# Optimization experiments

Hardware: AMD Instinct MI355X
Metric: run time of the kernel (lower is better)

The kernel has to match this reference:

```python
import jax, jax.numpy as jnp
import numpy as np

DIM = 256; WS = 8; HEADS = 8; HD = DIM // HEADS; SCALE = HD ** -0.5; MLP_HIDDEN = 1024
B = 8; H = 128; W = 128


def setup_inputs() -> dict:
    key = jax.random.key(0)
    ks = jax.random.split(key, 16)
    def nrm(k, shape, s=0.02):
        return jax.random.normal(k, shape, jnp.float32) * s
    # relative position index (same construction as torch buffer)
    coords = np.stack(np.meshgrid(np.arange(WS), np.arange(WS), indexing='ij')).reshape(2, -1)
    rel = (coords[:, :, None] - coords[:, None, :]).transpose(1, 2, 0).astype(np.int64)
    rel[..., 0] += WS - 1; rel[..., 1] += WS - 1; rel[..., 0] *= 2 * WS - 1
    rel_idx = jnp.asarray(rel.sum(-1), jnp.int32)  # (64,64) in [0,225)
    return dict(
        x=nrm(ks[0], (B, H, W, DIM), 1.0),
        rel_table=nrm(ks[1], ((2 * WS - 1) ** 2, HEADS)),
        qkv_w=nrm(ks[2], (3 * DIM, DIM)), qkv_b=nrm(ks[3], (3 * DIM,)),
        qkv2_w=nrm(ks[4], (3 * DIM, DIM)), qkv2_b=nrm(ks[5], (3 * DIM,)),
        proj_ln_w=jnp.ones((DIM,), jnp.float32), proj_ln_b=jnp.zeros((DIM,), jnp.float32),
        proj_w=nrm(ks[6], (DIM, DIM)), proj_b=nrm(ks[7], (DIM,)),
        proj2_ln_w=jnp.ones((DIM,), jnp.float32), proj2_ln_b=jnp.zeros((DIM,), jnp.float32),
        proj2_w=nrm(ks[8], (DIM, DIM)), proj2_b=nrm(ks[9], (DIM,)),
        norm1_w=jnp.ones((DIM,), jnp.float32), norm1_b=jnp.zeros((DIM,), jnp.float32),
        norm2_w=jnp.ones((DIM,), jnp.float32), norm2_b=jnp.zeros((DIM,), jnp.float32),
        fc1_w=nrm(ks[10], (MLP_HIDDEN, DIM)), fc1_b=nrm(ks[11], (MLP_HIDDEN,)),
        fc2_w=nrm(ks[12], (DIM, MLP_HIDDEN)), fc2_b=nrm(ks[13], (DIM,)),
        rel_idx=rel_idx,
    )


def _ln(x, w, b):
    mu = x.mean(-1, keepdims=True)
    var = ((x - mu) ** 2).mean(-1, keepdims=True)
    return (x - mu) / jnp.sqrt(var + 1e-5) * w + b


def _mha(tokens, wqkv, bqkv, bias=None):
    Bt, N, C = tokens.shape
    qkv = (tokens @ wqkv.T + bqkv).reshape(Bt, N, 3, HEADS, HD).transpose(2, 0, 3, 1, 4)
    q, k, v = qkv[0] * SCALE, qkv[1], qkv[2]
    attn = jnp.einsum('bhnd,bhmd->bhnm', q, k)
    if bias is not None:
        attn = attn + bias  # (1,heads,N,N) relative position bias
    attn = jax.nn.softmax(attn, axis=-1)
    out = jnp.einsum('bhnm,bhmd->bhnd', attn, v)
    return out.transpose(0, 2, 1, 3).reshape(Bt, N, C)


def _pos_sine(h, w, c):
    # PositionEmbeddingSine(normalize=True), mask all-zero -> cumsum = 1..h / 1..w
    npf = c // 2
    scale = 2.0 * np.pi; eps = 1e-5
    y = jnp.arange(1, h + 1, dtype=jnp.float32); y = y / (y[-1] + eps) * scale
    xw = jnp.arange(1, w + 1, dtype=jnp.float32); xw = xw / (xw[-1] + eps) * scale
    dim_t = 10000.0 ** ((2.0 * (jnp.arange(npf) // 2)) / npf)
    def enc(e):  # (L,) -> (L,npf) interleaved sin/cos
        p = e[:, None] / dim_t
        return jnp.stack([jnp.sin(p[:, 0::2]), jnp.cos(p[:, 1::2])], axis=-1).reshape(e.shape[0], npf)
    py = enc(y); px = enc(xw)
    return jnp.concatenate([jnp.broadcast_to(py[:, None, :], (h, w, npf)),
                            jnp.broadcast_to(px[None, :, :], (h, w, npf))], axis=-1)  # (h,w,c)


def _upsample_ac(x, oh, ow):
    # bilinear, align_corners=True; x: (B,h,w,C)
    Bn, h, w, C = x.shape
    def idx(n, o):
        s = jnp.linspace(0.0, n - 1.0, o)
        i0 = jnp.floor(s).astype(jnp.int32)
        i1 = jnp.minimum(i0 + 1, n - 1)
        return i0, i1, s - i0
    y0, y1, ty = idx(h, oh)
    x = x[:, y0] * (1 - ty)[None, :, None, None] + x[:, y1] * ty[None, :, None, None]
    x0, x1, tx = idx(w, ow)
    x = x[:, :, x0] * (1 - tx)[None, None, :, None] + x[:, :, x1] * tx[None, None, :, None]
    return x


def reference(x, rel_table, qkv_w, qkv_b, qkv2_w, qkv2_b,
              proj_ln_w, proj_ln_b, proj_w, proj_b,
              proj2_ln_w, proj2_ln_b, proj2_w, proj2_b,
              norm1_w, norm1_b, norm2_w, norm2_b,
              fc1_w, fc1_b, fc2_w, fc2_b, rel_idx):
    Bn, Hh, Ww, C = x.shape  # H,W divisible by WS -> padding is a no-op
    nh, nw = Hh // WS, Ww // WS
    N = WS * WS
    shortcut = x
    # window partition -> (B*nh*nw, N, C)
    xw = x.reshape(Bn, nh, WS, nw, WS, C).transpose(0, 1, 3, 2, 4, 5).reshape(-1, N, C)
    bias = rel_table[rel_idx.reshape(-1)].reshape(N, N, HEADS).transpose(2, 0, 1)[None]
    xw = _mha(xw, qkv_w, qkv_b, bias)
    xw = xw.reshape(Bn, nh, nw, WS, WS, C).transpose(0, 1, 3, 2, 4, 5).reshape(Bn, Hh, Ww, C)
    x = shortcut + xw
    x = x + (_ln(x, proj_ln_w, proj_ln_b) @ proj_w.T + proj_b)
    shortcut = x
    # global branch: avgpool each window, sine pos enc, full attention, bilinear upsample
    xg = x.reshape(Bn, nh, WS, nw, WS, C).mean(axis=(2, 4))  # (B,nh,nw,C)
    xg = xg + _pos_sine(nh, nw, C)[None]
    xg = _mha(xg.reshape(Bn, nh * nw, C), qkv2_w, qkv2_b).reshape(Bn, nh, nw, C)
    xg = _upsample_ac(xg, Hh, Ww)
    x = shortcut + xg
    x = x + (_ln(x, proj2_ln_w, proj2_ln_b) @ proj2_w.T + proj2_b)
    h = _ln(x, norm1_w, norm1_b)
    h = jax.nn.gelu(h @ fc1_w.T + fc1_b, approximate=False) @ fc2_w.T + fc2_b
    x = x + h
    return _ln(x, norm2_w, norm2_b)
```

## Files before the change

### kernel.cpp

```cpp
#include <hip/hip_runtime.h>
#include <math.h>

#define DEV __device__ __forceinline__

constexpr int NTOK = 131072;
constexpr int TOKS_PER_B = 16384;
constexpr float SCALE_F = 0.17677669529663687f;

typedef float f32x4 __attribute__((ext_vector_type(4)));
typedef __bf16 bf16x8 __attribute__((ext_vector_type(8)));
typedef unsigned short us8 __attribute__((ext_vector_type(8)));

DEV float gelu1(float v) { return 0.5f * v * (1.f + erff(v * 0.7071067811865476f)); }
DEV unsigned short f2bf(float x) { __bf16 b = (__bf16)x; return __builtin_bit_cast(unsigned short, b); }
DEV float bfh2f(unsigned short h) { return __builtin_bit_cast(float, ((unsigned)h) << 16); }

__global__ void cvtw_k(const float* __restrict__ w, unsigned short* __restrict__ dst, int n) {
  const int i = (blockIdx.x * 256 + threadIdx.x) * 4;
  float4 v = *(const float4*)(w + i);
  ushort4 h, l;
  h.x = f2bf(v.x); l.x = f2bf(v.x - bfh2f(h.x));
  h.y = f2bf(v.y); l.y = f2bf(v.y - bfh2f(h.y));
  h.z = f2bf(v.z); l.z = f2bf(v.z - bfh2f(h.z));
  h.w = f2bf(v.w); l.w = f2bf(v.w - bfh2f(h.w));
  *(ushort4*)(dst + i) = h;
  *(ushort4*)(dst + n + i) = l;
}

template <bool LNA, bool RES, bool GELU>
__launch_bounds__(256)
__global__ void gemm_mfma(const float* __restrict__ A, const unsigned short* __restrict__ Wp,
                          const float* __restrict__ bias, float* out,
                          const float* __restrict__ stats,
                          const float* __restrict__ lnw, const float* __restrict__ lnb,
                          int M, int N, int K) {
  __shared__ unsigned short Ah[64][40], Al[64][40];
  __shared__ unsigned short Wh[256][40], Wl[256][40];
  const int t = threadIdx.x;
  const int lane = t & 63, wid = t >> 6;
  const int m0 = blockIdx.x * 64, n0 = blockIdx.y * 256;
  const unsigned short* Whp = Wp;
  const unsigned short* Wlp = Wp + (size_t)N * K;

  f32x4 acc[4][4];
#pragma unroll
  for (int i = 0; i < 4; ++i)
#pragma unroll
    for (int j = 0; j < 4; ++j) acc[i][j] = (f32x4){0.f, 0.f, 0.f, 0.f};

  const int fr = lane & 15, ko = (lane >> 4) * 8;

  for (int k0 = 0; k0 < K; k0 += 32) {
#pragma unroll
    for (int it = 0; it < 2; ++it) {
      const int id = t + it * 256;
      const int r = id >> 3, cg = id & 7;
      float4 v = *(const float4*)(A + (size_t)(m0 + r) * K + k0 + cg * 4);
      if (LNA) {
        const float mu = stats[(size_t)(m0 + r) * 2];
        const float rs = stats[(size_t)(m0 + r) * 2 + 1];
        float4 w4 = *(const float4*)(lnw + k0 + cg * 4);
        float4 b4 = *(const float4*)(lnb + k0 + cg * 4);
        v.x = (v.x - mu) * rs * w4.x + b4.x; v.y = (v.y - mu) * rs * w4.y + b4.y;
        v.z = (v.z - mu) * rs * w4.z + b4.z; v.w = (v.w - mu) * rs * w4.w + b4.w;
      }
      ushort4 h, l;
      h.x = f2bf(v.x); l.x = f2bf(v.x - bfh2f(h.x));
      h.y = f2bf(v.y); l.y = f2bf(v.y - bfh2f(h.y));
      h.z = f2bf(v.z); l.z = f2bf(v.z - bfh2f(h.z));
      h.w = f2bf(v.w); l.w = f2bf(v.w - bfh2f(h.w));
      *(ushort4*)&Ah[r][cg * 4] = h;
      *(ushort4*)&Al[r][cg * 4] = l;
    }
#pragma unroll
    for (int it = 0; it < 4; ++it) {
      const int id = t + it * 256;
      const int rn = id >> 2, kc = (id & 3) * 8;
      const size_t goff = (size_t)(n0 + rn) * K + k0 + kc;
      *(us8*)&Wh[rn][kc] = *(const us8*)(Whp + goff);
      *(us8*)&Wl[rn][kc] = *(const us8*)(Wlp + goff);
    }
    __syncthreads();
    bf16x8 ah[4], al[4], bh[4], bl[4];
#pragma unroll
    for (int i = 0; i < 4; ++i) {
      ah[i] = __builtin_bit_cast(bf16x8, *(const us8*)&Ah[i * 16 + fr][ko]);
      al[i] = __builtin_bit_cast(bf16x8, *(const us8*)&Al[i * 16 + fr][ko]);
      bh[i] = __builtin_bit_cast(bf16x8, *(const us8*)&Wh[wid * 64 + i * 16 + fr][ko]);
      bl[i] = __builtin_bit_cast(bf16x8, *(const us8*)&Wl[wid * 64 + i * 16 + fr][ko]);
    }
#pragma unroll
    for (int i = 0; i < 4; ++i)
#pragma unroll
      for (int j = 0; j < 4; ++j) {
        acc[i][j] = __builtin_amdgcn_mfma_f32_16x16x32_bf16(ah[i], bh[j], acc[i][j], 0, 0, 0);
        acc[i][j] = __builtin_amdgcn_mfma_f32_16x16x32_bf16(ah[i], bl[j], acc[i][j], 0, 0, 0);
        acc[i][j] = __builtin_amdgcn_mfma_f32_16x16x32_bf16(al[i], bh[j], acc[i][j], 0, 0, 0);
      }
    __syncthreads();
  }
  const int orow = (lane >> 4) * 4;
#pragma unroll
  for (int i = 0; i < 4; ++i)
#pragma unroll
    for (int j = 0; j < 4; ++j) {
      const int col = n0 + wid * 64 + j * 16 + fr;
      const float b = bias[col];
#pragma unroll
      for (int r = 0; r < 4; ++r) {
        const int row = m0 + i * 16 + orow + r;
        float v = acc[i][j][r] + b;
        if (GELU) v = gelu1(v);
        float* p = out + (size_t)row * N + col;
        if (RES) v += *p;
        *p = v;
      }
    }
}

__global__ void winattn_k(const float* __restrict__ qkv, const float* __restrict__ xin,
                          float* __restrict__ X, const float* __restrict__ rel_table,
                          const int* __restrict__ rel_idx, int b0) {
  __shared__ float klds[64][36];
  __shared__ float vlds[64][36];
  const int b_rel = blockIdx.x >> 11;
  const int rest = blockIdx.x & 2047;
  const int widx = rest >> 3, h = rest & 7;
  const int wy = widx >> 4, wx = widx & 15;
  const int r = threadIdx.x;
  const int tl = (wy * 8 + (r >> 3)) * 128 + wx * 8 + (r & 7);
  const float* qr = qkv + ((size_t)b_rel * TOKS_PER_B + tl) * 768 + h * 32;
  float q[32];
#pragma unroll
  for (int j4 = 0; j4 < 8; ++j4) {
    float4 v = *(const float4*)(qr + j4 * 4);
    q[j4*4+0] = v.x * SCALE_F; q[j4*4+1] = v.y * SCALE_F;
    q[j4*4+2] = v.z * SCALE_F; q[j4*4+3] = v.w * SCALE_F;
  }
#pragma unroll
  for (int j4 = 0; j4 < 8; ++j4) {
    *(float4*)&klds[r][j4 * 4] = *(const float4*)(qr + 256 + j4 * 4);
    *(float4*)&vlds[r][j4 * 4] = *(const float4*)(qr + 512 + j4 * 4);
  }
  __syncthreads();
  float s[64];
  const int* ri = rel_idx + r * 64;
#pragma unroll
  for (int m = 0; m < 64; ++m) {
    float acc = 0.f;
#pragma unroll
    for (int j4 = 0; j4 < 8; ++j4) {
      float4 k4 = *(const float4*)&klds[m][j4 * 4];
      acc += q[j4*4+0]*k4.x + q[j4*4+1]*k4.y + q[j4*4+2]*k4.z + q[j4*4+3]*k4.w;
    }
    s[m] = acc + rel_table[ri[m] * 8 + h];
  }
  float mx = s[0];
#pragma unroll
  for (int m = 1; m < 64; ++m) mx = fmaxf(mx, s[m]);
  float sum = 0.f;
#pragma unroll
  for (int m = 0; m < 64; ++m) { s[m] = __expf(s[m] - mx); sum += s[m]; }
  const float inv = 1.f / sum;
  float o[32];
#pragma unroll
  for (int j = 0; j < 32; ++j) o[j] = 0.f;
#pragma unroll
  for (int m = 0; m < 64; ++m) {
    const float p = s[m];
#pragma unroll
    for (int j4 = 0; j4 < 8; ++j4) {
      float4 v4 = *(const float4*)&vlds[m][j4 * 4];
      o[j4*4+0] += p * v4.x; o[j4*4+1] += p * v4.y;
      o[j4*4+2] += p * v4.z; o[j4*4+3] += p * v4.w;
    }
  }
  const size_t go = (size_t)((b0 + b_rel) * TOKS_PER_B + tl) * 256 + h * 32;
#pragma unroll
  for (int j4 = 0; j4 < 8; ++j4) {
    float4 xi = *(const float4*)(xin + go + j4 * 4);
    float4 rr;
    rr.x = o[j4*4+0] * inv + xi.x; rr.y = o[j4*4+1] * inv + xi.y;
    rr.z = o[j4*4+2] * inv + xi.z; rr.w = o[j4*4+3] * inv + xi.w;
    *(float4*)(X + go + j4 * 4) = rr;
  }
}

__global__ void lnstats_k(const float* __restrict__ X, float* __restrict__ stats) {
  const int lane = threadIdx.x & 63;
  const int wave = threadIdx.x >> 6;
  for (int tok = blockIdx.x * 4 + wave; tok < NTOK; tok += gridDim.x * 4) {
    float4 v = *(const float4*)(X + (size_t)tok * 256 + lane * 4);
    float s = v.x + v.y + v.z + v.w;
    float q = v.x*v.x + v.y*v.y + v.z*v.z + v.w*v.w;
#pragma unroll
    for (int off = 32; off > 0; off >>= 1) {
      s += __shfl_xor(s, off, 64);
      q += __shfl_xor(q, off, 64);
    }
    if (lane == 0) {
      const float m = s * (1.f / 256.f);
      const float var = q * (1.f / 256.f) - m * m;
      stats[(size_t)tok * 2] = m;
      stats[(size_t)tok * 2 + 1] = 1.f / sqrtf(var + 1e-5f);
    }
  }
}

__global__ void finalln_k(float* X, const float* __restrict__ w, const float* __restrict__ b) {
  const int lane = threadIdx.x & 63;
  const int wave = threadIdx.x >> 6;
  for (int tok = blockIdx.x * 4 + wave; tok < NTOK; tok += gridDim.x * 4) {
    float* p = X + (size_t)tok * 256 + lane * 4;
    float4 v = *(const float4*)p;
    float s = v.x + v.y + v.z + v.w;
    float q = v.x*v.x + v.y*v.y + v.z*v.z + v.w*v.w;
#pragma unroll
    for (int off = 32; off > 0; off >>= 1) {
      s += __shfl_xor(s, off, 64);
      q += __shfl_xor(q, off, 64);
    }
    const float m = s * (1.f / 256.f);
    const float var = q * (1.f / 256.f) - m * m;
    const float rs = 1.f / sqrtf(var + 1e-5f);
    float4 w4 = *(const float4*)(w + lane * 4);
    float4 b4 = *(const float4*)(b + lane * 4);
    v.x = (v.x - m) * rs * w4.x + b4.x; v.y = (v.y - m) * rs * w4.y + b4.y;
    v.z = (v.z - m) * rs * w4.z + b4.z; v.w = (v.w - m) * rs * w4.w + b4.w;
    *(float4*)p = v;
  }
}

__global__ void poolsine_k(const float* __restrict__ X, float* __restrict__ G0) {
  const int c = threadIdx.x;
  const int wx = blockIdx.x & 15, wy = (blockIdx.x >> 4) & 15, b = blockIdx.x >> 8;
  const float* base = X + ((size_t)(b * 128 + wy * 8) * 128 + wx * 8) * 256 + c;
  float s = 0.f;
  for (int ry = 0; ry < 8; ++ry)
#pragma unroll
    for (int rx = 0; rx < 8; ++rx) s += base[((size_t)ry * 128 + rx) * 256];
  s *= (1.f / 64.f);
  const float sc = 6.283185307179586f / (16.f + 1e-5f);
  const int cc = c & 127;
  const float d = powf(10000.f, (float)(cc >> 1) * (1.f / 64.f));
  const float e = ((c < 128 ? (float)(wy + 1) : (float)(wx + 1)) * sc) / d;
  const float pos = (cc & 1) ? cosf(e) : sinf(e);
  G0[(size_t)blockIdx.x * 256 + c] = s + pos;
}

__global__ void gattn_k(const float* __restrict__ G1, float* __restrict__ G2) {
  const int b = blockIdx.x, h = blockIdx.y, n = threadIdx.x;
  const float* qp = G1 + ((size_t)b * 256 + n) * 768 + h * 32;
  float q[32];
#pragma unroll
  for (int j4 = 0; j4 < 8; ++j4) {
    float4 v = *(const float4*)(qp + j4 * 4);
    q[j4*4+0] = v.x * SCALE_F; q[j4*4+1] = v.y * SCALE_F;
    q[j4*4+2] = v.z * SCALE_F; q[j4*4+3] = v.w * SCALE_F;
  }
  const float* kb = G1 + (size_t)b * 256 * 768 + 256 + h * 32;
  const float* vb = kb + 256;
  float out[32];
#pragma unroll
  for (int j = 0; j < 32; ++j) out[j] = 0.f;
  float mx = -3.4e38f, l = 0.f;
  for (int m = 0; m < 256; ++m) {
    const float* kr = kb + (size_t)m * 768;
    float s = 0.f;
#pragma unroll
    for (int j4 = 0; j4 < 8; ++j4) {
      float4 k4 = *(const float4*)(kr + j4 * 4);
      s += q[j4*4+0]*k4.x + q[j4*4+1]*k4.y + q[j4*4+2]*k4.z + q[j4*4+3]*k4.w;
    }
    const float mn = fmaxf(mx, s);
    const float corr = __expf(mx - mn);
    const float p = __expf(s - mn);
    l = l * corr + p;
    const float* vr = vb + (size_t)m * 768;
#pragma unroll
    for (int j4 = 0; j4 < 8; ++j4) {
      float4 v4 = *(const float4*)(vr + j4 * 4);
      out[j4*4+0] = out[j4*4+0]*corr + p*v4.x; out[j4*4+1] = out[j4*4+1]*corr + p*v4.y;
      out[j4*4+2] = out[j4*4+2]*corr + p*v4.z; out[j4*4+3] = out[j4*4+3]*corr + p*v4.w;
    }
    mx = mn;
  }
  const float inv = 1.f / l;
  float* op = G2 + ((size_t)b * 256 + n) * 256 + h * 32;
#pragma unroll
  for (int j4 = 0; j4 < 8; ++j4) {
    float4 r;
    r.x = out[j4*4+0]*inv; r.y = out[j4*4+1]*inv;
    r.z = out[j4*4+2]*inv; r.w = out[j4*4+3]*inv;
    *(float4*)(op + j4 * 4) = r;
  }
}

__global__ void upadd_k(float* __restrict__ X, const float* __restrict__ G2,
                        float* __restrict__ stats) {
  const int c = threadIdx.x;
  const int tok = blockIdx.x;
  const int j = tok & 127, i = (tok >> 7) & 127, b = tok >> 14;
  const float sy = i * (15.f / 127.f);
  const float sx = j * (15.f / 127.f);
  const int y0 = (int)sy; const float ty = sy - y0; const int y1 = min(y0 + 1, 15);
  const int x0 = (int)sx; const float tx = sx - x0; const int x1 = min(x0 + 1, 15);
  const float* gb = G2 + (size_t)b * 256 * 256;
  const float v00 = gb[((size_t)(y0 * 16 + x0)) * 256 + c];
  const float v01 = gb[((size_t)(y0 * 16 + x1)) * 256 + c];
  const float v10 = gb[((size_t)(y1 * 16 + x0)) * 256 + c];
  const float v11 = gb[((size_t)(y1 * 16 + x1)) * 256 + c];
  const float vy0 = v00 * (1.f - ty) + v10 * ty;
  const float vy1 = v01 * (1.f - ty) + v11 * ty;
  const float val = X[(size_t)tok * 256 + c] + vy0 * (1.f - tx) + vy1 * tx;
  X[(size_t)tok * 256 + c] = val;
  float s = val, q = val * val;
#pragma unroll
  for (int off = 32; off > 0; off >>= 1) {
    s += __shfl_xor(s, off, 64);
    q += __shfl_xor(q, off, 64);
  }
  __shared__ float red[8];
  const int lane = c & 63, wave = c >> 6;
  if (lane == 0) { red[wave * 2] = s; red[wave * 2 + 1] = q; }
  __syncthreads();
  if (c == 0) {
    const float S = red[0] + red[2] + red[4] + red[6];
    const float Q = red[1] + red[3] + red[5] + red[7];
    const float m = S * (1.f / 256.f);
    const float var = Q * (1.f / 256.f) - m * m;
    stats[(size_t)tok * 2] = m;
    stats[(size_t)tok * 2 + 1] = 1.f / sqrtf(var + 1e-5f);
  }
}

extern "C" void kernel_launch(void* const* d_in, const int* in_sizes, int n_in,
                              void* d_out, int out_size, void* d_ws, size_t ws_size,
                              hipStream_t stream) {
  const float* x          = (const float*)d_in[0];
  const float* rel_table  = (const float*)d_in[1];
  const float* qkv_w      = (const float*)d_in[2];
  const float* qkv_b      = (const float*)d_in[3];
  const float* qkv2_w     = (const float*)d_in[4];
  const float* qkv2_b     = (const float*)d_in[5];
  const float* proj_ln_w  = (const float*)d_in[6];
  const float* proj_ln_b  = (const float*)d_in[7];
  const float* proj_w     = (const float*)d_in[8];
  const float* proj_b     = (const float*)d_in[9];
  const float* proj2_ln_w = (const float*)d_in[10];
  const float* proj2_ln_b = (const float*)d_in[11];
  const float* proj2_w    = (const float*)d_in[12];
  const float* proj2_b    = (const float*)d_in[13];
  const float* norm1_w    = (const float*)d_in[14];
  const float* norm1_b    = (const float*)d_in[15];
  const float* norm2_w    = (const float*)d_in[16];
  const float* norm2_b    = (const float*)d_in[17];
  const float* fc1_w      = (const float*)d_in[18];
  const float* fc1_b      = (const float*)d_in[19];
  const float* fc2_w      = (const float*)d_in[20];
  const float* fc2_b      = (const float*)d_in[21];
  const int*   rel_idx    = (const int*)d_in[22];

  float* X = (float*)d_out;
  char* wsb = (char*)d_ws;
  float* stats = (float*)wsb;
  float* G0 = (float*)(wsb + (size_t)1048576);
  float* G1 = G0 + (size_t)2048 * 256;
  float* G2 = G1 + (size_t)2048 * 768;
  unsigned short* WCVT = (unsigned short*)(G2 + (size_t)2048 * 256);
  float* BIG = (float*)((char*)WCVT + (size_t)4194304);
  const size_t fixed = (size_t)((char*)BIG - wsb);
  const size_t avail = ws_size > fixed ? ws_size - fixed : 0;

  unsigned short* w_qkv  = WCVT;
  unsigned short* w_qkv2 = WCVT + 393216;
  unsigned short* w_proj = WCVT + 786432;
  unsigned short* w_proj2= WCVT + 917504;
  unsigned short* w_fc1  = WCVT + 1048576;
  unsigned short* w_fc2  = WCVT + 1572864;
  cvtw_k<<<192, 256, 0, stream>>>(qkv_w,   w_qkv,   196608);
  cvtw_k<<<192, 256, 0, stream>>>(qkv2_w,  w_qkv2,  196608);
  cvtw_k<<<64,  256, 0, stream>>>(proj_w,  w_proj,   65536);
  cvtw_k<<<64,  256, 0, stream>>>(proj2_w, w_proj2,  65536);
  cvtw_k<<<256, 256, 0, stream>>>(fc1_w,   w_fc1,   262144);
  cvtw_k<<<256, 256, 0, stream>>>(fc2_w,   w_fc2,   262144);

  int st = 8192;
  if (avail >= (size_t)65536 * 1024 * 4) st = 65536;
  else if (avail >= (size_t)32768 * 1024 * 4) st = 32768;
  else if (avail >= (size_t)16384 * 1024 * 4) st = 16384;
  const bool one_shot_qkv = avail >= (size_t)NTOK * 768 * 4;

  if (one_shot_qkv) {
    gemm_mfma<false, false, false><<<dim3(NTOK / 64, 3), 256, 0, stream>>>(
        x, w_qkv, qkv_b, BIG, nullptr, nullptr, nullptr, NTOK, 768, 256);
    winattn_k<<<16384, 64, 0, stream>>>(BIG, x, X, rel_table, rel_idx, 0);
  } else {
    for (int b = 0; b < 8; ++b) {
      gemm_mfma<false, false, false><<<dim3(TOKS_PER_B / 64, 3), 256, 0, stream>>>(
          x + (size_t)b * TOKS_PER_B * 256, w_qkv, qkv_b, BIG,
          nullptr, nullptr, nullptr, TOKS_PER_B, 768, 256);
      winattn_k<<<2048, 64, 0, stream>>>(BIG, x, X, rel_table, rel_idx, b);
    }
  }
  lnstats_k<<<1024, 256, 0, stream>>>(X, stats);
  gemm_mfma<true, true, false><<<dim3(NTOK / 64, 1), 256, 0, stream>>>(
      X, w_proj, proj_b, X, stats, proj_ln_w, proj_ln_b, NTOK, 256, 256);
  poolsine_k<<<2048, 256, 0, stream>>>(X, G0);
  gemm_mfma<false, false, false><<<dim3(32, 3), 256, 0, stream>>>(
      G0, w_qkv2, qkv2_b, G1, nullptr, nullptr, nullptr, 2048, 768, 256);
  gattn_k<<<dim3(8, 8), 256, 0, stream>>>(G1, G2);
  upadd_k<<<NTOK, 256, 0, stream>>>(X, G2, stats);
  gemm_mfma<true, true, false><<<dim3(NTOK / 64, 1), 256, 0, stream>>>(
      X, w_proj2, proj2_b, X, stats, proj2_ln_w, proj2_ln_b, NTOK, 256, 256);
  lnstats_k<<<1024, 256, 0, stream>>>(X, stats);
  for (int s0 = 0; s0 < NTOK; s0 += st) {
    gemm_mfma<true, false, true><<<dim3(st / 64, 4), 256, 0, stream>>>(
        X + (size_t)s0 * 256, w_fc1, fc1_b, BIG, stats + (size_t)s0 * 2,
        norm1_w, norm1_b, st, 1024, 256);
    gemm_mfma<false, true, false><<<dim3(st / 64, 1), 256, 0, stream>>>(
        BIG, w_fc2, fc2_b, X + (size_t)s0 * 256, nullptr, nullptr, nullptr,
        st, 256, 1024);
  }
  finalln_k<<<1024, 256, 0, stream>>>(X, norm2_w, norm2_b);
}
```

Before: 2.129 ms.

## Switch GEMMs to fp16 split-weight MFMA and store intermediates in half

Replaces the three-pass bf16 hi/lo split GEMM with fp16 MFMA that uses a single fp16 activation and split fp16 weights, so each tile needs two MFMAs instead of three and one A staging buffer instead of two. The QKV and fc1 intermediate buffers are now written in fp16, which halves the traffic of the large intermediates and lets fc2 read half-precision A directly. Window attention now packs four windows per 256-thread block and reads fp16 K/V from LDS, and the fc chunk size grows because the buffers are smaller. The risks are lower accuracy from rounding activations to fp16 (range and precision) and possible overflow of the fp16 intermediates.

Result: slower. 2.408 ms (+13.1%).

```diff
diff --git a/kernel.cpp b/kernel.cpp
--- a/kernel.cpp
+++ b/kernel.cpp
@@ -8,38 +8,37 @@
 constexpr float SCALE_F = 0.17677669529663687f;
 
 typedef float f32x4 __attribute__((ext_vector_type(4)));
-typedef __bf16 bf16x8 __attribute__((ext_vector_type(8)));
+typedef _Float16 half8 __attribute__((ext_vector_type(8)));
 typedef unsigned short us8 __attribute__((ext_vector_type(8)));
 
 DEV float gelu1(float v) { return 0.5f * v * (1.f + erff(v * 0.7071067811865476f)); }
-DEV unsigned short f2bf(float x) { __bf16 b = (__bf16)x; return __builtin_bit_cast(unsigned short, b); }
-DEV float bfh2f(unsigned short h) { return __builtin_bit_cast(float, ((unsigned)h) << 16); }
-
-__global__ void cvtw_k(const float* __restrict__ w, unsigned short* __restrict__ dst, int n) {
+DEV unsigned short f2h(float x) { _Float16 h = (_Float16)x; return __builtin_bit_cast(unsigned short, h); }
+DEV float h2f(unsigned short u) { return (float)__builtin_bit_cast(_Float16, u); }
+
+__global__ void cvtw16_k(const float* __restrict__ w, unsigned short* __restrict__ dst, int n) {
   const int i = (blockIdx.x * 256 + threadIdx.x) * 4;
   float4 v = *(const float4*)(w + i);
   ushort4 h, l;
-  h.x = f2bf(v.x); l.x = f2bf(v.x - bfh2f(h.x));
-  h.y = f2bf(v.y); l.y = f2bf(v.y - bfh2f(h.y));
-  h.z = f2bf(v.z); l.z = f2bf(v.z - bfh2f(h.z));
-  h.w = f2bf(v.w); l.w = f2bf(v.w - bfh2f(h.w));
+  h.x = f2h(v.x); l.x = f2h(v.x - h2f(h.x));
+  h.y = f2h(v.y); l.y = f2h(v.y - h2f(h.y));
+  h.z = f2h(v.z); l.z = f2h(v.z - h2f(h.z));
+  h.w = f2h(v.w); l.w = f2h(v.w - h2f(h.w));
   *(ushort4*)(dst + i) = h;
   *(ushort4*)(dst + n + i) = l;
 }
 
-template <bool LNA, bool RES, bool GELU>
+template <int AMODE, bool RES, bool GELU, bool OUTH>
 __launch_bounds__(256)
-__global__ void gemm_mfma(const float* __restrict__ A, const unsigned short* __restrict__ Wp,
-                          const float* __restrict__ bias, float* out,
-                          const float* __restrict__ stats,
-                          const float* __restrict__ lnw, const float* __restrict__ lnb,
-                          int M, int N, int K) {
-  __shared__ unsigned short Ah[64][40], Al[64][40];
+__global__ void gemm16(const void* __restrict__ Ain, const unsigned short* __restrict__ Wp,
+                       const float* __restrict__ bias, void* __restrict__ outv,
+                       const float* __restrict__ stats,
+                       const float* __restrict__ lnw, const float* __restrict__ lnb,
+                       int M, int N, int K) {
+  __shared__ unsigned short As[64][40];
   __shared__ unsigned short Wh[256][40], Wl[256][40];
   const int t = threadIdx.x;
   const int lane = t & 63, wid = t >> 6;
   const int m0 = blockIdx.x * 64, n0 = blockIdx.y * 256;
-  const unsigned short* Whp = Wp;
   const unsigned short* Wlp = Wp + (size_t)N * K;
 
   f32x4 acc[4][4];
@@ -49,98 +48,106 @@
     for (int j = 0; j < 4; ++j) acc[i][j] = (f32x4){0.f, 0.f, 0.f, 0.f};
 
   const int fr = lane & 15, ko = (lane >> 4) * 8;
+  const int ar = t >> 2, ac = (t & 3) * 8;
+  float mu = 0.f, rs = 1.f;
+  if (AMODE == 1) {
+    mu = stats[(size_t)(m0 + ar) * 2];
+    rs = stats[(size_t)(m0 + ar) * 2 + 1];
+  }
 
   for (int k0 = 0; k0 < K; k0 += 32) {
-#pragma unroll
-    for (int it = 0; it < 2; ++it) {
-      const int id = t + it * 256;
-      const int r = id >> 3, cg = id & 7;
-      float4 v = *(const float4*)(A + (size_t)(m0 + r) * K + k0 + cg * 4);
-      if (LNA) {
-        const float mu = stats[(size_t)(m0 + r) * 2];
-        const float rs = stats[(size_t)(m0 + r) * 2 + 1];
-        float4 w4 = *(const float4*)(lnw + k0 + cg * 4);
-        float4 b4 = *(const float4*)(lnb + k0 + cg * 4);
-        v.x = (v.x - mu) * rs * w4.x + b4.x; v.y = (v.y - mu) * rs * w4.y + b4.y;
-        v.z = (v.z - mu) * rs * w4.z + b4.z; v.w = (v.w - mu) * rs * w4.w + b4.w;
+    if (AMODE == 2) {
+      *(us8*)&As[ar][ac] =
+          *(const us8*)((const unsigned short*)Ain + (size_t)(m0 + ar) * K + k0 + ac);
+    } else {
+      const float* Af = (const float*)Ain;
+      float4 v0 = *(const float4*)(Af + (size_t)(m0 + ar) * K + k0 + ac);
+      float4 v1 = *(const float4*)(Af + (size_t)(m0 + ar) * K + k0 + ac + 4);
+      if (AMODE == 1) {
+        float4 w0 = *(const float4*)(lnw + k0 + ac), w1 = *(const float4*)(lnw + k0 + ac + 4);
+        float4 b0 = *(const float4*)(lnb + k0 + ac), b1 = *(const float4*)(lnb + k0 + ac + 4);
+        v0.x = (v0.x - mu) * rs * w0.x + b0.x;  v0.y = (v0.y - mu) * rs * w0.y + b0.y;
+        v0.z = (v0.z - mu) * rs * w0.z + b0.z;  v0.w = (v0.w - mu) * rs * w0.w + b0.w;
+        v1.x = (v1.x - mu) * rs * w1.x + b1.x;  v1.y = (v1.y - mu) * rs * w1.y + b1.y;
+        v1.z = (v1.z - mu) * rs * w1.z + b1.z;  v1.w = (v1.w - mu) * rs * w1.w + b1.w;
       }
-      ushort4 h, l;
-      h.x = f2bf(v.x); l.x = f2bf(v.x - bfh2f(h.x));
-      h.y = f2bf(v.y); l.y = f2bf(v.y - bfh2f(h.y));
-      h.z = f2bf(v.z); l.z = f2bf(v.z - bfh2f(h.z));
-      h.w = f2bf(v.w); l.w = f2bf(v.w - bfh2f(h.w));
-      *(ushort4*)&Ah[r][cg * 4] = h;
-      *(ushort4*)&Al[r][cg * 4] = l;
+      us8 hh;
+      hh[0] = f2h(v0.x); hh[1] = f2h(v0.y); hh[2] = f2h(v0.z); hh[3] = f2h(v0.w);
+      hh[4] = f2h(v1.x); hh[5] = f2h(v1.y); hh[6] = f2h(v1.z); hh[7] = f2h(v1.w);
+      *(us8*)&As[ar][ac] = hh;
     }
 #pragma unroll
     for (int it = 0; it < 4; ++it) {
       const int id = t + it * 256;
       const int rn = id >> 2, kc = (id & 3) * 8;
-      const size_t goff = (size_t)(n0 + rn) * K + k0 + kc;
-      *(us8*)&Wh[rn][kc] = *(const us8*)(Whp + goff);
-      *(us8*)&Wl[rn][kc] = *(const us8*)(Wlp + goff);
+      const size_t g = (size_t)(n0 + rn) * K + k0 + kc;
+      *(us8*)&Wh[rn][kc] = *(const us8*)(Wp + g);
+      *(us8*)&Wl[rn][kc] = *(const us8*)(Wlp + g);
     }
     __syncthreads();
-    bf16x8 ah[4], al[4], bh[4], bl[4];
+    half8 a4[4], bh4[4], bl4[4];
 #pragma unroll
     for (int i = 0; i < 4; ++i) {
-      ah[i] = __builtin_bit_cast(bf16x8, *(const us8*)&Ah[i * 16 + fr][ko]);
-      al[i] = __builtin_bit_cast(bf16x8, *(const us8*)&Al[i * 16 + fr][ko]);
-      bh[i] = __builtin_bit_cast(bf16x8, *(const us8*)&Wh[wid * 64 + i * 16 + fr][ko]);
-      bl[i] = __builtin_bit_cast(bf16x8, *(const us8*)&Wl[wid * 64 + i * 16 + fr][ko]);
+      a4[i] = __builtin_bit_cast(half8, *(const us8*)&As[i * 16 + fr][ko]);
+      bh4[i] = __builtin_bit_cast(half8, *(const us8*)&Wh[wid * 64 + i * 16 + fr][ko]);
+      bl4[i] = __builtin_bit_cast(half8, *(const us8*)&Wl[wid * 64 + i * 16 + fr][ko]);
     }
 #pragma unroll
     for (int i = 0; i < 4; ++i)
 #pragma unroll
       for (int j = 0; j < 4; ++j) {
-        acc[i][j] = __builtin_amdgcn_mfma_f32_16x16x32_bf16(ah[i], bh[j], acc[i][j], 0, 0, 0);
-        acc[i][j] = __builtin_amdgcn_mfma_f32_16x16x32_bf16(ah[i], bl[j], acc[i][j], 0, 0, 0);
-        acc[i][j] = __builtin_amdgcn_mfma_f32_16x16x32_bf16(al[i], bh[j], acc[i][j], 0, 0, 0);
+        acc[i][j] = __builtin_amdgcn_mfma_f32_16x16x32_f16(a4[i], bh4[j], acc[i][j], 0, 0, 0);
+        acc[i][j] = __builtin_amdgcn_mfma_f32_16x16x32_f16(a4[i], bl4[j], acc[i][j], 0, 0, 0);
       }
     __syncthreads();
   }
-  const int orow = (lane >> 4) * 4;
+  const int or4 = (lane >> 4) * 4;
 #pragma unroll
   for (int i = 0; i < 4; ++i)
 #pragma unroll
     for (int j = 0; j < 4; ++j) {
       const int col = n0 + wid * 64 + j * 16 + fr;
-      const float b = bias[col];
-#pragma unroll
-      for (int r = 0; r < 4; ++r) {
-        const int row = m0 + i * 16 + orow + r;
-        float v = acc[i][j][r] + b;
+      const float bb = bias[col];
+#pragma unroll
+      for (int r4 = 0; r4 < 4; ++r4) {
+        const int row = m0 + i * 16 + or4 + r4;
+        float v = acc[i][j][r4] + bb;
         if (GELU) v = gelu1(v);
-        float* p = out + (size_t)row * N + col;
-        if (RES) v += *p;
-        *p = v;
+        if (OUTH) {
+          ((unsigned short*)outv)[(size_t)row * N + col] = f2h(v);
+        } else {
+          float* p = (float*)outv + (size_t)row * N + col;
+          if (RES) v += *p;
+          *p = v;
+        }
       }
     }
 }
 
-__global__ void winattn_k(const float* __restrict__ qkv, const float* __restrict__ xin,
+__launch_bounds__(256)
+__global__ void winattn_k(const unsigned short* __restrict__ qkv, const float* __restrict__ xin,
                           float* __restrict__ X, const float* __restrict__ rel_table,
                           const int* __restrict__ rel_idx, int b0) {
-  __shared__ float klds[64][36];
-  __shared__ float vlds[64][36];
-  const int b_rel = blockIdx.x >> 11;
-  const int rest = blockIdx.x & 2047;
+  __shared__ unsigned short klds[4][64][40];
+  __shared__ unsigned short vlds[4][64][40];
+  const int wid = threadIdx.x >> 6, r = threadIdx.x & 63;
+  const int p = blockIdx.x * 4 + wid;
+  const int brel = p >> 11, rest = p & 2047;
   const int widx = rest >> 3, h = rest & 7;
   const int wy = widx >> 4, wx = widx & 15;
-  const int r = threadIdx.x;
   const int tl = (wy * 8 + (r >> 3)) * 128 + wx * 8 + (r & 7);
-  const float* qr = qkv + ((size_t)b_rel * TOKS_PER_B + tl) * 768 + h * 32;
+  const unsigned short* qr = qkv + ((size_t)brel * TOKS_PER_B + tl) * 768 + h * 32;
   float q[32];
 #pragma unroll
-  for (int j4 = 0; j4 < 8; ++j4) {
-    float4 v = *(const float4*)(qr + j4 * 4);
-    q[j4*4+0] = v.x * SCALE_F; q[j4*4+1] = v.y * SCALE_F;
-    q[j4*4+2] = v.z * SCALE_F; q[j4*4+3] = v.w * SCALE_F;
-  }
-#pragma unroll
-  for (int j4 = 0; j4 < 8; ++j4) {
-    *(float4*)&klds[r][j4 * 4] = *(const float4*)(qr + 256 + j4 * 4);
-    *(float4*)&vlds[r][j4 * 4] = *(const float4*)(qr + 512 + j4 * 4);
+  for (int j = 0; j < 4; ++j) {
+    us8 qq = *(const us8*)(qr + j * 8);
+#pragma unroll
+    for (int e = 0; e < 8; ++e) q[j * 8 + e] = h2f(qq[e]) * SCALE_F;
+  }
+#pragma unroll
+  for (int j = 0; j < 4; ++j) {
+    *(us8*)&klds[wid][r][j * 8] = *(const us8*)(qr + 256 + j * 8);
+    *(us8*)&vlds[wid][r][j * 8] = *(const us8*)(qr + 512 + j * 8);
   }
   __syncthreads();
   float s[64];
@@ -149,9 +156,10 @@
   for (int m = 0; m < 64; ++m) {
     float acc = 0.f;
 #pragma unroll
-    for (int j4 = 0; j4 < 8; ++j4) {
-      float4 k4 = *(const float4*)&klds[m][j4 * 4];
-      acc += q[j4*4+0]*k4.x + q[j4*4+1]*k4.y + q[j4*4+2]*k4.z + q[j4*4+3]*k4.w;
+    for (int j = 0; j < 4; ++j) {
+      us8 kw = *(const us8*)&klds[wid][m][j * 8];
+#pragma unroll
+      for (int e = 0; e < 8; ++e) acc += q[j * 8 + e] * h2f(kw[e]);
     }
     s[m] = acc + rel_table[ri[m] * 8 + h];
   }
@@ -167,15 +175,15 @@
   for (int j = 0; j < 32; ++j) o[j] = 0.f;
 #pragma unroll
   for (int m = 0; m < 64; ++m) {
-    const float p = s[m];
-#pragma unroll
-    for (int j4 = 0; j4 < 8; ++j4) {
-      float4 v4 = *(const float4*)&vlds[m][j4 * 4];
-      o[j4*4+0] += p * v4.x; o[j4*4+1] += p * v4.y;
-      o[j4*4+2] += p * v4.z; o[j4*4+3] += p * v4.w;
-    }
-  }
-  const size_t go = (size_t)((b0 + b_rel) * TOKS_PER_B + tl) * 256 + h * 32;
+    const float pm = s[m];
+#pragma unroll
+    for (int j = 0; j < 4; ++j) {
+      us8 vw = *(const us8*)&vlds[wid][m][j * 8];
+#pragma unroll
+      for (int e = 0; e < 8; ++e) o[j * 8 + e] += pm * h2f(vw[e]);
+    }
+  }
+  const size_t go = (size_t)((b0 + brel) * TOKS_PER_B + tl) * 256 + h * 32;
 #pragma unroll
   for (int j4 = 0; j4 < 8; ++j4) {
     float4 xi = *(const float4*)(xin + go + j4 * 4);
@@ -368,8 +376,9 @@
   float* G1 = G0 + (size_t)2048 * 256;
   float* G2 = G1 + (size_t)2048 * 768;
   unsigned short* WCVT = (unsigned short*)(G2 + (size_t)2048 * 256);
-  float* BIG = (float*)((char*)WCVT + (size_t)4194304);
-  const size_t fixed = (size_t)((char*)BIG - wsb);
+  char* BIG = (char*)WCVT + (size_t)4194304;
+  unsigned short* BIGH = (unsigned short*)BIG;
+  const size_t fixed = (size_t)(BIG - wsb);
   const size_t avail = ws_size > fixed ? ws_size - fixed : 0;
 
   unsigned short* w_qkv  = WCVT;
@@ -378,48 +387,48 @@
   unsigned short* w_proj2= WCVT + 917504;
   unsigned short* w_fc1  = WCVT + 1048576;
   unsigned short* w_fc2  = WCVT + 1572864;
-  cvtw_k<<<192, 256, 0, stream>>>(qkv_w,   w_qkv,   196608);
-  cvtw_k<<<192, 256, 0, stream>>>(qkv2_w,  w_qkv2,  196608);
-  cvtw_k<<<64,  256, 0, stream>>>(proj_w,  w_proj,   65536);
-  cvtw_k<<<64,  256, 0, stream>>>(proj2_w, w_proj2,  65536);
-  cvtw_k<<<256, 256, 0, stream>>>(fc1_w,   w_fc1,   262144);
-  cvtw_k<<<256, 256, 0, stream>>>(fc2_w,   w_fc2,   262144);
-
-  int st = 8192;
-  if (avail >= (size_t)65536 * 1024 * 4) st = 65536;
-  else if (avail >= (size_t)32768 * 1024 * 4) st = 32768;
-  else if (avail >= (size_t)16384 * 1024 * 4) st = 16384;
-  const bool one_shot_qkv = avail >= (size_t)NTOK * 768 * 4;
-
-  if (one_shot_qkv) {
-    gemm_mfma<false, false, false><<<dim3(NTOK / 64, 3), 256, 0, stream>>>(
-        x, w_qkv, qkv_b, BIG, nullptr, nullptr, nullptr, NTOK, 768, 256);
-    winattn_k<<<16384, 64, 0, stream>>>(BIG, x, X, rel_table, rel_idx, 0);
+  cvtw16_k<<<192, 256, 0, stream>>>(qkv_w,   w_qkv,   196608);
+  cvtw16_k<<<192, 256, 0, stream>>>(qkv2_w,  w_qkv2,  196608);
+  cvtw16_k<<<64,  256, 0, stream>>>(proj_w,  w_proj,   65536);
+  cvtw16_k<<<64,  256, 0, stream>>>(proj2_w, w_proj2,  65536);
+  cvtw16_k<<<256, 256, 0, stream>>>(fc1_w,   w_fc1,   262144);
+  cvtw16_k<<<256, 256, 0, stream>>>(fc2_w,   w_fc2,   262144);
+
+  int st = 16384;
+  if (avail >= (size_t)268435456) st = 131072;
+  else if (avail >= (size_t)134217728) st = 65536;
+  else if (avail >= (size_t)67108864) st = 32768;
+  const bool one_shot = avail >= (size_t)NTOK * 768 * 2;
+
+  if (one_shot) {
+    gemm16<0, false, false, true><<<dim3(NTOK / 64, 3), 256, 0, stream>>>(
+        x, w_qkv, qkv_b, BIGH, nullptr, nullptr, nullptr, NTOK, 768, 256);
+    winattn_k<<<4096, 256, 0, stream>>>(BIGH, x, X, rel_table, rel_idx, 0);
   } else {
     for (int b = 0; b < 8; ++b) {
-      gemm_mfma<false, false, false><<<dim3(TOKS_PER_B / 64, 3), 256, 0, stream>>>(
-          x + (size_t)b * TOKS_PER_B * 256, w_qkv, qkv_b, BIG,
+      gemm16<0, false, false, true><<<dim3(TOKS_PER_B / 64, 3), 256, 0, stream>>>(
+          x + (size_t)b * TOKS_PER_B * 256, w_qkv, qkv_b, BIGH,
           nullptr, nullptr, nullptr, TOKS_PER_B, 768, 256);
-      winattn_k<<<2048, 64, 0, stream>>>(BIG, x, X, rel_table, rel_idx, b);
+      winattn_k<<<512, 256, 0, stream>>>(BIGH, x, X, rel_table, rel_idx, b);
     }
   }
   lnstats_k<<<1024, 256, 0, stream>>>(X, stats);
-  gemm_mfma<true, true, false><<<dim3(NTOK / 64, 1), 256, 0, stream>>>(
+  gemm16<1, true, false, false><<<dim3(NTOK / 64, 1), 256, 0, stream>>>(
       X, w_proj, proj_b, X, stats, proj_ln_w, proj_ln_b, NTOK, 256, 256);
   poolsine_k<<<2048, 256, 0, stream>>>(X, G0);
-  gemm_mfma<false, false, false><<<dim3(32, 3), 256, 0, stream>>>(
+  gemm16<0, false, false, false><<<dim3(32, 3), 256, 0, stream>>>(
       G0, w_qkv2, qkv2_b, G1, nullptr, nullptr, nullptr, 2048, 768, 256);
   gattn_k<<<dim3(8, 8), 256, 0, stream>>>(G1, G2);
   upadd_k<<<NTOK, 256, 0, stream>>>(X, G2, stats);
-  gemm_mfma<true, true, false><<<dim3(NTOK / 64, 1), 256, 0, stream>>>(
+  gemm16<1, true, false, false><<<dim3(NTOK / 64, 1), 256, 0, stream>>>(
       X, w_proj2, proj2_b, X, stats, proj2_ln_w, proj2_ln_b, NTOK, 256, 256);
   lnstats_k<<<1024, 256, 0, stream>>>(X, stats);
   for (int s0 = 0; s0 < NTOK; s0 += st) {
-    gemm_mfma<true, false, true><<<dim3(st / 64, 4), 256, 0, stream>>>(
-        X + (size_t)s0 * 256, w_fc1, fc1_b, BIG, stats + (size_t)s0 * 2,
+    gemm16<1, false, true, true><<<dim3(st / 64, 4), 256, 0, stream>>>(
+        X + (size_t)s0 * 256, w_fc1, fc1_b, BIGH, stats + (size_t)s0 * 2,
         norm1_w, norm1_b, st, 1024, 256);
-    gemm_mfma<false, true, false><<<dim3(st / 64, 1), 256, 0, stream>>>(
-        BIG, w_fc2, fc2_b, X + (size_t)s0 * 256, nullptr, nullptr, nullptr,
+    gemm16<2, true, false, false><<<dim3(st / 64, 1), 256, 0, stream>>>(
+        BIGH, w_fc2, fc2_b, X + (size_t)s0 * 256, nullptr, nullptr, nullptr,
         st, 256, 1024);
   }
   finalln_k<<<1024, 256, 0, stream>>>(X, norm2_w, norm2_b);
```
